# Kernel tuning notes

Measured on AMD Instinct MI355X. Metric: run time of the kernel, lower is better.

## Reference

```python
import jax, jax.numpy as jnp
import numpy as np

WORLD_SIZE = 8
NUM_FEATURES = 8   # num_my_features (local tables on this rank)
BATCH = 4096
EMB_ROWS = 200000
EMB_DIM = 64
MAX_POOL = 128     # per-bag lengths drawn from [0, MAX_POOL)


def _exclusive_cumsum(x):
    # lengthsToOffsets: cumsum(cat([0], lengths[:-1]))
    c = jnp.cumsum(x)
    return jnp.concatenate([jnp.zeros((1,), x.dtype), c[:-1]])


def setup_inputs() -> dict:
    key = jax.random.key(0)
    k1, k2, k3 = jax.random.split(key, 3)
    n_bags = WORLD_SIZE * NUM_FEATURES * BATCH
    lengths = jax.random.randint(k1, (n_bags,), 0, MAX_POOL, dtype=jnp.int32)
    total = int(jnp.sum(lengths))  # concrete at setup time -> static shape
    indices = jax.random.randint(k2, (total,), 0, EMB_ROWS, dtype=jnp.int32)
    emb = jax.random.normal(k3, (NUM_FEATURES, EMB_ROWS, EMB_DIM), dtype=jnp.float32) * 0.01
    return {"lengths": lengths, "indices": indices, "emb": emb}


def _split_per_table(lengths, indices):
    """Vectorized, fused equivalent of paramDLRM_Net.splitPerTable.

    Input bags are laid out in (rank, feature, batch) order; the op regroups
    them into per-feature streams, i.e. (feature, rank, batch) order, and
    rebuilds per-feature offsets from the regrouped lengths.
    """
    R, F, B = WORLD_SIZE, NUM_FEATURES, BATCH
    T = indices.shape[0]
    n_bags = R * F * B
    # output bag -> input bag permutation: (f, r, b) <- (r, f, b)
    perm = jnp.arange(n_bags, dtype=jnp.int32).reshape(R, F, B).transpose(1, 0, 2).reshape(-1)
    off_in = _exclusive_cumsum(lengths)          # start of each input bag in `indices`
    L_out = lengths[perm]                        # regrouped lengths, (f, r, b) order
    start_out = off_in[perm]
    off_out = _exclusive_cumsum(L_out)           # global exclusive offsets in output order
    starts = jnp.repeat(start_out, L_out, total_repeat_length=T)
    bag_of_elem = jnp.repeat(jnp.arange(n_bags, dtype=jnp.int32), L_out, total_repeat_length=T)
    within = jnp.arange(T, dtype=jnp.int32) - jnp.repeat(off_out, L_out, total_repeat_length=T)
    permuted = indices[starts + within]          # all_feature_indices, concatenated over features
    off2d = off_out.reshape(F, R * B)
    offsets = off2d - off2d[:, :1]               # per-feature offsets restart at 0 (lengthsToOffsets)
    return offsets, permuted, bag_of_elem


def reference(lengths, indices, emb):
    F = NUM_FEATURES
    RB = WORLD_SIZE * BATCH
    offsets, permuted, bag_of_elem = _split_per_table(lengths, indices)
    # apply_emb: per-feature EmbeddingBag (sum mode) over the regrouped jagged indices
    feat = bag_of_elem // RB                     # which table each element belongs to
    rows = emb[feat, permuted]                   # [T, D] gathered embedding rows
    ly = jax.ops.segment_sum(rows, bag_of_elem, num_segments=F * RB).reshape(F, RB, EMB_DIM)
    return offsets, permuted, ly
```

## Files before the change

kernel.cpp:

```cpp
#include <hip/hip_runtime.h>

#define R_WS 8
#define F_NF 8
#define B_BATCH 4096
#define EMB_ROWS 200000
#define EMB_DIM 64
#define NBAGS (R_WS * F_NF * B_BATCH)
#define RB_SZ (R_WS * B_BATCH)
#define SCAN_NB 256
#define SCAN_BT 256
#define SCAN_ITEMS 4

typedef float vfloat4 __attribute__((ext_vector_type(4)));

__device__ __forceinline__ int perm_src(int o) {
    int f  = o >> 15;
    int rb = o & (RB_SZ - 1);
    int r  = rb >> 12;
    int b2 = rb & (B_BATCH - 1);
    return (r << 15) + (f << 12) + b2;
}

__global__ __launch_bounds__(SCAN_BT) void scan_pass1(
        const int* __restrict__ lengths, int* __restrict__ bsums) {
    int b = blockIdx.x, t = threadIdx.x;
    int base = b * (SCAN_BT * SCAN_ITEMS) + t * SCAN_ITEMS;
    int s_in = 0, s_out = 0;
#pragma unroll
    for (int k = 0; k < SCAN_ITEMS; ++k) {
        s_in  += lengths[base + k];
        s_out += lengths[perm_src(base + k)];
    }
    __shared__ int lin[SCAN_BT], lout[SCAN_BT];
    lin[t] = s_in; lout[t] = s_out;
    __syncthreads();
    for (int d = SCAN_BT / 2; d > 0; d >>= 1) {
        if (t < d) { lin[t] += lin[t + d]; lout[t] += lout[t + d]; }
        __syncthreads();
    }
    if (t == 0) { bsums[b] = lin[0]; bsums[SCAN_NB + b] = lout[0]; }
}

__global__ __launch_bounds__(SCAN_BT) void scan_pass2(int* __restrict__ bsums) {
    int t = threadIdx.x;
    __shared__ int s[2 * SCAN_NB];
    int o1 = bsums[t], o2 = bsums[SCAN_NB + t];
    s[t] = o1; s[SCAN_NB + t] = o2;
    __syncthreads();
    for (int d = 1; d < SCAN_NB; d <<= 1) {
        int a = (t >= d) ? s[t - d] : 0;
        int c = (t >= d) ? s[SCAN_NB + t - d] : 0;
        __syncthreads();
        s[t] += a; s[SCAN_NB + t] += c;
        __syncthreads();
    }
    bsums[t] = s[t] - o1;
    bsums[SCAN_NB + t] = s[SCAN_NB + t] - o2;
}

__global__ __launch_bounds__(SCAN_BT) void scan_pass3(
        const int* __restrict__ lengths, const int* __restrict__ bsums,
        int* __restrict__ off_in, int* __restrict__ off_out) {
    int b = blockIdx.x, t = threadIdx.x;
    int base = b * (SCAN_BT * SCAN_ITEMS) + t * SCAN_ITEMS;
    int vin[SCAN_ITEMS], vout[SCAN_ITEMS];
    int tin = 0, tout = 0;
#pragma unroll
    for (int k = 0; k < SCAN_ITEMS; ++k) {
        vin[k]  = lengths[base + k];
        vout[k] = lengths[perm_src(base + k)];
        tin += vin[k]; tout += vout[k];
    }
    __shared__ int sin_[SCAN_BT], sout_[SCAN_BT];
    sin_[t] = tin; sout_[t] = tout;
    __syncthreads();
    for (int d = 1; d < SCAN_BT; d <<= 1) {
        int a = (t >= d) ? sin_[t - d] : 0;
        int c = (t >= d) ? sout_[t - d] : 0;
        __syncthreads();
        sin_[t] += a; sout_[t] += c;
        __syncthreads();
    }
    int ebase_in  = sin_[t]  - tin  + bsums[b];
    int ebase_out = sout_[t] - tout + bsums[SCAN_NB + b];
    int run_i = 0, run_o = 0;
#pragma unroll
    for (int k = 0; k < SCAN_ITEMS; ++k) {
        off_in[base + k]  = ebase_in + run_i;  run_i += vin[k];
        off_out[base + k] = ebase_out + run_o; run_o += vout[k];
    }
}

__global__ __launch_bounds__(256) void bag_kernel(
        const int* __restrict__ lengths, const int* __restrict__ indices,
        const float* __restrict__ emb,
        const int* __restrict__ off_in, const int* __restrict__ off_out,
        float* __restrict__ out_offsets, float* __restrict__ out_permuted,
        float* __restrict__ out_ly) {
    int wid  = (int)((blockIdx.x * blockDim.x + threadIdx.x) >> 6);
    int lane = threadIdx.x & 63;
    if (wid >= NBAGS) return;
    int o = wid;
    int f = o >> 15;
    int src = perm_src(o);
    int start = off_in[src];
    int len   = lengths[src];
    int obase = off_out[o];
    if (lane == 0)
        out_offsets[o] = (float)(obase - off_out[f << 15]);
    const float* etab = emb + (size_t)f * ((size_t)EMB_ROWS * EMB_DIM);
    int g = lane >> 4;
    int s = lane & 15;
    float ax = 0.f, ay = 0.f, az = 0.f, aw = 0.f;
    for (int j0 = 0; j0 < len; j0 += 64) {
        int rem = len - j0;
        int n = rem < 64 ? rem : 64;
        int idx = 0;
        if (lane < n) {
            idx = __builtin_nontemporal_load(&indices[start + j0 + lane]);
            __builtin_nontemporal_store((float)idx, &out_permuted[obase + j0 + lane]);
        }
        if (n == 64) {
#pragma unroll 8
            for (int jj = 0; jj < 16; ++jj) {
                int row = __shfl(idx, jj * 4 + g, 64);
                const vfloat4* p = (const vfloat4*)(etab + (size_t)row * EMB_DIM + s * 4);
                vfloat4 v = *p;
                ax += v.x; ay += v.y; az += v.z; aw += v.w;
            }
        } else {
            int nj = (n + 3) >> 2;
            for (int jj = 0; jj < nj; ++jj) {
                int k = jj * 4 + g;
                int row = __shfl(idx, k, 64);
                if (k < n) {
                    const vfloat4* p = (const vfloat4*)(etab + (size_t)row * EMB_DIM + s * 4);
                    vfloat4 v = *p;
                    ax += v.x; ay += v.y; az += v.z; aw += v.w;
                }
            }
        }
    }
    ax += __shfl_xor(ax, 16, 64); ay += __shfl_xor(ay, 16, 64);
    az += __shfl_xor(az, 16, 64); aw += __shfl_xor(aw, 16, 64);
    ax += __shfl_xor(ax, 32, 64); ay += __shfl_xor(ay, 32, 64);
    az += __shfl_xor(az, 32, 64); aw += __shfl_xor(aw, 32, 64);
    if (lane < 16) {
        vfloat4 r; r.x = ax; r.y = ay; r.z = az; r.w = aw;
        __builtin_nontemporal_store(r, (vfloat4*)(out_ly + (size_t)o * EMB_DIM + s * 4));
    }
}

extern "C" void kernel_launch(void* const* d_in, const int* in_sizes, int n_in,
                              void* d_out, int out_size, void* d_ws, size_t ws_size,
                              hipStream_t stream) {
    const int*   lengths = (const int*)d_in[0];
    const int*   indices = (const int*)d_in[1];
    const float* emb     = (const float*)d_in[2];
    int T = in_sizes[1];

    int* off_in  = (int*)d_ws;
    int* off_out = off_in + NBAGS;
    int* bsums   = off_out + NBAGS;

    float* out          = (float*)d_out;
    float* out_offsets  = out;
    float* out_permuted = out + NBAGS;
    float* out_ly       = out_permuted + T;

    scan_pass1<<<SCAN_NB, SCAN_BT, 0, stream>>>(lengths, bsums);
    scan_pass2<<<1, SCAN_BT, 0, stream>>>(bsums);
    scan_pass3<<<SCAN_NB, SCAN_BT, 0, stream>>>(lengths, bsums, off_in, off_out);
    bag_kernel<<<NBAGS / 4, 256, 0, stream>>>(lengths, indices, emb, off_in, off_out,
                                              out_offsets, out_permuted, out_ly);
}
```

Before: 1.026 ms.

## Split embedding gather into two row-range passes for cache locality

The bag kernel now runs twice, each pass accumulating only indices that fall in half of the embedding row range. Out-of-range lookups are redirected to a fixed row and weighted by zero, and the second pass adds its result onto the first pass's output. The intent is to shrink the working set of random row gathers per pass so that it fits in the last-level cache. In exchange, all indices are reread and every load is issued twice, and the output is read back and rewritten.

New measurement: 1.164 ms. 1.13x slower.

```diff
diff --git a/kernel.cpp b/kernel.cpp
--- a/kernel.cpp
+++ b/kernel.cpp
@@ -10,6 +10,9 @@
 #define SCAN_NB 256
 #define SCAN_BT 256
 #define SCAN_ITEMS 4
+
+#define NPASS 2
+#define ROWS_PER_PASS (EMB_ROWS / NPASS)
 
 typedef float vfloat4 __attribute__((ext_vector_type(4)));
 
@@ -96,7 +99,7 @@
         const float* __restrict__ emb,
         const int* __restrict__ off_in, const int* __restrict__ off_out,
         float* __restrict__ out_offsets, float* __restrict__ out_permuted,
-        float* __restrict__ out_ly) {
+        float* __restrict__ out_ly, int pass) {
     int wid  = (int)((blockIdx.x * blockDim.x + threadIdx.x) >> 6);
     int lane = threadIdx.x & 63;
     if (wid >= NBAGS) return;
@@ -106,9 +109,10 @@
     int start = off_in[src];
     int len   = lengths[src];
     int obase = off_out[o];
-    if (lane == 0)
+    if (pass == 0 && lane == 0)
         out_offsets[o] = (float)(obase - off_out[f << 15]);
     const float* etab = emb + (size_t)f * ((size_t)EMB_ROWS * EMB_DIM);
+    const int lo = pass * ROWS_PER_PASS;
     int g = lane >> 4;
     int s = lane & 15;
     float ax = 0.f, ay = 0.f, az = 0.f, aw = 0.f;
@@ -118,26 +122,33 @@
         int idx = 0;
         if (lane < n) {
             idx = __builtin_nontemporal_load(&indices[start + j0 + lane]);
-            __builtin_nontemporal_store((float)idx, &out_permuted[obase + j0 + lane]);
+            if (pass == 0)
+                __builtin_nontemporal_store((float)idx, &out_permuted[obase + j0 + lane]);
         }
         if (n == 64) {
 #pragma unroll 8
             for (int jj = 0; jj < 16; ++jj) {
                 int row = __shfl(idx, jj * 4 + g, 64);
-                const vfloat4* p = (const vfloat4*)(etab + (size_t)row * EMB_DIM + s * 4);
+                bool inr = (unsigned)(row - lo) < (unsigned)ROWS_PER_PASS;
+                int rsel = inr ? row : lo;
+                const vfloat4* p = (const vfloat4*)(etab + (size_t)rsel * EMB_DIM + s * 4);
                 vfloat4 v = *p;
-                ax += v.x; ay += v.y; az += v.z; aw += v.w;
+                float w = inr ? 1.f : 0.f;
+                ax = fmaf(v.x, w, ax); ay = fmaf(v.y, w, ay);
+                az = fmaf(v.z, w, az); aw = fmaf(v.w, w, aw);
             }
         } else {
             int nj = (n + 3) >> 2;
             for (int jj = 0; jj < nj; ++jj) {
                 int k = jj * 4 + g;
                 int row = __shfl(idx, k, 64);
-                if (k < n) {
-                    const vfloat4* p = (const vfloat4*)(etab + (size_t)row * EMB_DIM + s * 4);
-                    vfloat4 v = *p;
-                    ax += v.x; ay += v.y; az += v.z; aw += v.w;
-                }
+                bool ok = (k < n) && ((unsigned)(row - lo) < (unsigned)ROWS_PER_PASS);
+                int rsel = ok ? row : lo;
+                const vfloat4* p = (const vfloat4*)(etab + (size_t)rsel * EMB_DIM + s * 4);
+                vfloat4 v = *p;
+                float w = ok ? 1.f : 0.f;
+                ax = fmaf(v.x, w, ax); ay = fmaf(v.y, w, ay);
+                az = fmaf(v.z, w, az); aw = fmaf(v.w, w, aw);
             }
         }
     }
@@ -147,7 +158,12 @@
     az += __shfl_xor(az, 32, 64); aw += __shfl_xor(aw, 32, 64);
     if (lane < 16) {
         vfloat4 r; r.x = ax; r.y = ay; r.z = az; r.w = aw;
-        __builtin_nontemporal_store(r, (vfloat4*)(out_ly + (size_t)o * EMB_DIM + s * 4));
+        vfloat4* dst = (vfloat4*)(out_ly + (size_t)o * EMB_DIM + s * 4);
+        if (pass != 0) {
+            vfloat4 old = __builtin_nontemporal_load(dst);
+            r.x += old.x; r.y += old.y; r.z += old.z; r.w += old.w;
+        }
+        __builtin_nontemporal_store(r, dst);
     }
 }
 
@@ -171,6 +187,7 @@
     scan_pass1<<<SCAN_NB, SCAN_BT, 0, stream>>>(lengths, bsums);
     scan_pass2<<<1, SCAN_BT, 0, stream>>>(bsums);
     scan_pass3<<<SCAN_NB, SCAN_BT, 0, stream>>>(lengths, bsums, off_in, off_out);
-    bag_kernel<<<NBAGS / 4, 256, 0, stream>>>(lengths, indices, emb, off_in, off_out,
-                                              out_offsets, out_permuted, out_ly);
+    for (int p = 0; p < NPASS; ++p)
+        bag_kernel<<<NBAGS / 4, 256, 0, stream>>>(lengths, indices, emb, off_in, off_out,
+                                                  out_offsets, out_permuted, out_ly, p);
 }
```
